# Performance work log

Measured on AMD Instinct MI355X. Metric: run time of the kernel, lower is better.

## Reference

```python
import jax, jax.numpy as jnp
import numpy as np
import math

D = 128  # hidden_dim
N_USERS = 10000
N_ITEMS = 12000
NEG_INF = -9e15


def setup_inputs() -> dict:
    key = jax.random.key(0)
    k1, k2, k3, k4, k5 = jax.random.split(key, 5)
    ufea = jax.random.normal(k1, (N_USERS, D), dtype=jnp.float32)
    inter = jax.random.normal(k2, (N_ITEMS, D), dtype=jnp.float32)
    adj = jax.random.randint(k3, (N_USERS, N_ITEMS), 0, 2, dtype=jnp.int32)
    # linear layer params (torch default init approximated with scaled normals)
    W = jax.random.normal(k4, (D, D), dtype=jnp.float32) / jnp.sqrt(jnp.float32(D))
    b = jax.random.normal(k5, (D,), dtype=jnp.float32) * 0.01
    return {"ufea": ufea, "inter": inter, "adj": adj, "W": W, "b": b}


def _leaky_relu2(x):
    # nn.LeakyReLU(2): negative_slope = 2
    return jnp.where(x > 0, x, 2.0 * x)


def reference(ufea, inter, adj, W, b):
    # GAT.forward_user with dropout in eval mode (identity).
    # Attention.forward(a=ufea, b=inter, adj)
    query = ufea @ W.T + b                      # [N, D]  nn.Linear
    scale = 1.0 / math.sqrt(D)
    scores = _leaky_relu2((query @ inter.T) * scale)   # [N, M]
    scores = jnp.where(adj > 0, scores, NEG_INF)        # mask non-edges
    attn = jax.nn.softmax(scores, axis=1)               # row softmax
    result = attn @ inter                                # [N, D]
    return result
```

## Files before the change

kernel.cpp:

```cpp
#include <hip/hip_runtime.h>
#include <cstdint>
#include <cstddef>


#define N_USERS 10000
#define N_ITEMS 12000
#define HD      128
#define QROWS   10112
#define NCHUNK  9
#define TILE    64
#define NTILES  188
#define UBLOCKS 79
#define QBLOCKS 632

typedef __bf16 bf16x8 __attribute__((ext_vector_type(8)));
typedef __bf16 bf16x4 __attribute__((ext_vector_type(4)));
typedef float  f32x4  __attribute__((ext_vector_type(4)));
typedef int    i32x4  __attribute__((ext_vector_type(4)));

typedef const __attribute__((address_space(1))) unsigned int g_u32;
typedef __attribute__((address_space(3))) unsigned int l_u32;

__global__ __launch_bounds__(256) void prep_kernel(const float* __restrict__ inter,
                                                   const float* __restrict__ ufea,
                                                   const float* __restrict__ W,
                                                   const float* __restrict__ bias,
                                                   __bf16* __restrict__ kvg,
                                                   __bf16* __restrict__ qg) {
    __shared__ __bf16 Tl[128 * 72];
    const int t = threadIdx.x;
    const int lane = t & 63, wave = t >> 6;
    const int n = lane & 15, qd = lane >> 4;

    if (blockIdx.x < NTILES) {
        const int tile = blockIdx.x;
        const int i0 = tile * 64;
        for (int it = 0; it < 8; ++it) {
            int g   = it * 256 + t;
            int row = g >> 5;
            int d   = (g & 31) * 4;
            int item = i0 + row;
            if (item < N_ITEMS) {
                f32x4 v = *(const f32x4*)(inter + (size_t)item * HD + d);
                Tl[(d + 0) * 72 + row] = (__bf16)v.x;
                Tl[(d + 1) * 72 + row] = (__bf16)v.y;
                Tl[(d + 2) * 72 + row] = (__bf16)v.z;
                Tl[(d + 3) * 72 + row] = (__bf16)v.w;
            } else {
                Tl[(d + 0) * 72 + row] = (__bf16)0.f;
                Tl[(d + 1) * 72 + row] = (__bf16)0.f;
                Tl[(d + 2) * 72 + row] = (__bf16)0.f;
                Tl[(d + 3) * 72 + row] = (__bf16)0.f;
            }
        }
        __syncthreads();
        __bf16* tbase = kvg + (size_t)tile * (32 * 512);
        #pragma unroll
        for (int j = 0; j < 4; ++j) {
            const int c = wave * 4 + j;
            int row = i0 + 4 * n + wave;
            bf16x8 o;
            if (row < N_ITEMS) {
                const float* p = inter + (size_t)row * HD + j * 32 + qd * 8;
                f32x4 lo = *(const f32x4*)p, hi = *(const f32x4*)(p + 4);
                o[0]=(__bf16)lo.x; o[1]=(__bf16)lo.y; o[2]=(__bf16)lo.z; o[3]=(__bf16)lo.w;
                o[4]=(__bf16)hi.x; o[5]=(__bf16)hi.y; o[6]=(__bf16)hi.z; o[7]=(__bf16)hi.w;
            } else {
                #pragma unroll
                for (int e = 0; e < 8; ++e) o[e] = (__bf16)0.f;
            }
            *(bf16x8*)(tbase + (size_t)c * 512 + lane * 8) = o;
        }
        #pragma unroll
        for (int j = 0; j < 4; ++j) {
            const int cc = wave * 4 + j;
            const int dt = cc >> 1, kc = cc & 1;
            bf16x8 v = *(const bf16x8*)&Tl[(dt * 16 + n) * 72 + kc * 32 + qd * 8];
            *(bf16x8*)(tbase + (size_t)(16 + cc) * 512 + lane * 8) = v;
        }
    } else {
        const int user0 = (blockIdx.x - NTILES) * 16;
        int arow = user0 + n; if (arow > N_USERS - 1) arow = N_USERS - 1;

        bf16x8 af[4];
        #pragma unroll
        for (int kk = 0; kk < 4; ++kk) {
            const float* p = ufea + (size_t)arow * HD + kk * 32 + qd * 8;
            f32x4 lo = *(const f32x4*)p, hi = *(const f32x4*)(p + 4);
            bf16x8 a;
            a[0]=(__bf16)lo.x; a[1]=(__bf16)lo.y; a[2]=(__bf16)lo.z; a[3]=(__bf16)lo.w;
            a[4]=(__bf16)hi.x; a[5]=(__bf16)hi.y; a[6]=(__bf16)hi.z; a[7]=(__bf16)hi.w;
            af[kk] = a;
        }
        #pragma unroll
        for (int h = 0; h < 2; ++h) {
            const int nt = wave * 2 + h;
            f32x4 acc = {0.f, 0.f, 0.f, 0.f};
            #pragma unroll
            for (int kk = 0; kk < 4; ++kk) {
                const float* p = W + (size_t)(nt * 16 + n) * HD + kk * 32 + qd * 8;
                f32x4 lo = *(const f32x4*)p, hi = *(const f32x4*)(p + 4);
                bf16x8 b;
                b[0]=(__bf16)lo.x; b[1]=(__bf16)lo.y; b[2]=(__bf16)lo.z; b[3]=(__bf16)lo.w;
                b[4]=(__bf16)hi.x; b[5]=(__bf16)hi.y; b[6]=(__bf16)hi.z; b[7]=(__bf16)hi.w;
                acc = __builtin_amdgcn_mfma_f32_16x16x32_bf16(af[kk], b, acc, 0, 0, 0);
            }
            const float bv = bias[nt * 16 + n];
            #pragma unroll
            for (int r = 0; r < 4; ++r) {
                int row = user0 + qd * 4 + r;
                qg[(size_t)row * HD + nt * 16 + n] = (__bf16)(acc[r] + bv);
            }
        }
    }
}

__global__ __launch_bounds__(256)
__attribute__((amdgpu_waves_per_eu(3)))
void fused_kernel(const __bf16* __restrict__ qg,
                  const __bf16* __restrict__ kvg,
                  const int* __restrict__ adj,
                  float* __restrict__ Opart,
                  float* __restrict__ lpart) {
    __shared__ __bf16 Kbuf[16 * 512];
    __shared__ __bf16 Vbuf[16 * 512];
    __shared__ __bf16 Pl[4][32 * 72];
    const int lane = threadIdx.x & 63, wave = threadIdx.x >> 6;
    const int n = lane & 15, qd = lane >> 4;
    const int user0 = blockIdx.y * 128 + wave * 32;
    const int chunk = blockIdx.x;
    const int t0 = (chunk * NTILES) / NCHUNK;
    const int t1 = ((chunk + 1) * NTILES) / NCHUNK;
    const float SC = (float)(1.4426950408889634 * 0.08838834764831845);

    bf16x8 qf[2][4];
    #pragma unroll
    for (int g = 0; g < 2; ++g)
        #pragma unroll
        for (int kk = 0; kk < 4; ++kk)
            qf[g][kk] = *(const bf16x8*)(qg + (size_t)(user0 + g * 16 + n) * HD + kk * 32 + qd * 8);

    f32x4 Oacc[2][8];
    #pragma unroll
    for (int g = 0; g < 2; ++g)
        #pragma unroll
        for (int dt = 0; dt < 8; ++dt) Oacc[g][dt] = (f32x4){0.f, 0.f, 0.f, 0.f};
    float lacc[2][4] = {{0.f,0.f,0.f,0.f},{0.f,0.f,0.f,0.f}};

    int adjOff[2][4];
    #pragma unroll
    for (int g = 0; g < 2; ++g)
        #pragma unroll
        for (int r = 0; r < 4; ++r) {
            int u = user0 + g * 16 + qd * 4 + r;
            if (u > N_USERS - 1) u = N_USERS - 1;
            adjOff[g][r] = u * N_ITEMS;
        }
    __bf16* pw = &Pl[wave][0];

    for (int T = t0; T < t1; ++T) {
        const int j0 = T * TILE;
        const __bf16* tb = kvg + (size_t)T * (32 * 512);

        __builtin_amdgcn_s_barrier();

        #pragma unroll
        for (int j = 0; j < 4; ++j) {
            const int c = wave * 4 + j;
            __builtin_amdgcn_global_load_lds((g_u32*)(tb + (size_t)c * 512 + lane * 8),
                                             (l_u32*)(&Kbuf[c * 512]), 16, 0, 0);
        }
        #pragma unroll
        for (int j = 0; j < 4; ++j) {
            const int c = wave * 4 + j;
            __builtin_amdgcn_global_load_lds((g_u32*)(tb + (size_t)(16 + c) * 512 + lane * 8),
                                             (l_u32*)(&Vbuf[c * 512]), 16, 0, 0);
        }
        i32x4 av[2][4];
        {
            int col4 = j0 + 4 * n;
            if (col4 > N_ITEMS - 4) col4 = N_ITEMS - 4;
            #pragma unroll
            for (int g = 0; g < 2; ++g)
                #pragma unroll
                for (int r = 0; r < 4; ++r)
                    av[g][r] = __builtin_nontemporal_load((const i32x4*)(adj + adjOff[g][r] + col4));
        }
        __syncthreads();

        unsigned m0 = 0, m1 = 0;
        #pragma unroll
        for (int r = 0; r < 4; ++r)
            #pragma unroll
            for (int nt = 0; nt < 4; ++nt) {
                m0 |= (unsigned)(av[0][r][nt] > 0) << (r * 4 + nt);
                m1 |= (unsigned)(av[1][r][nt] > 0) << (r * 4 + nt);
            }
        unsigned vnib = 0;
        #pragma unroll
        for (int nt = 0; nt < 4; ++nt)
            vnib |= (unsigned)(j0 + 4 * n + nt < N_ITEMS) << nt;
        const unsigned vrep = vnib * 0x1111u;
        m0 &= vrep; m1 &= vrep;

        #pragma unroll
        for (int g = 0; g < 2; ++g) {
            f32x4 S[4];
            #pragma unroll
            for (int nt = 0; nt < 4; ++nt) S[nt] = (f32x4){0.f, 0.f, 0.f, 0.f};
            #pragma unroll
            for (int nt = 0; nt < 4; ++nt) {
                #pragma unroll
                for (int kk = 0; kk < 4; ++kk) {
                    bf16x8 b = *(const bf16x8*)(&Kbuf[(nt * 4 + kk) * 512 + lane * 8]);
                    S[nt] = __builtin_amdgcn_mfma_f32_16x16x32_bf16(qf[g][kk], b, S[nt], 0, 0, 0);
                }
            }
            const unsigned mg = g ? m1 : m0;
            #pragma unroll
            for (int r = 0; r < 4; ++r) {
                bf16x4 pk;
                #pragma unroll
                for (int nt = 0; nt < 4; ++nt) {
                    float s = S[nt][r] * SC;
                    s = fminf(s, s + s);
                    const bool on = (mg >> (r * 4 + nt)) & 1u;
                    float p = on ? __builtin_amdgcn_exp2f(s) : 0.f;
                    lacc[g][r] += p;
                    pk[nt] = (__bf16)p;
                }
                *(bf16x4*)(pw + (g * 16 + qd * 4 + r) * 72 + 4 * n) = pk;
            }
        }

        #pragma unroll
        for (int kc = 0; kc < 2; ++kc) {
            bf16x8 af0 = *(const bf16x8*)(pw + (0 * 16 + n) * 72 + kc * 32 + qd * 8);
            bf16x8 af1 = *(const bf16x8*)(pw + (1 * 16 + n) * 72 + kc * 32 + qd * 8);
            #pragma unroll
            for (int dt = 0; dt < 8; ++dt) {
                bf16x8 b = *(const bf16x8*)(&Vbuf[(dt * 2 + kc) * 512 + lane * 8]);
                Oacc[0][dt] = __builtin_amdgcn_mfma_f32_16x16x32_bf16(af0, b, Oacc[0][dt], 0, 0, 0);
                Oacc[1][dt] = __builtin_amdgcn_mfma_f32_16x16x32_bf16(af1, b, Oacc[1][dt], 0, 0, 0);
            }
        }
    }

    #pragma unroll
    for (int g = 0; g < 2; ++g)
        #pragma unroll
        for (int r = 0; r < 4; ++r) {
            float v = lacc[g][r];
            v += __shfl_xor(v, 1);
            v += __shfl_xor(v, 2);
            v += __shfl_xor(v, 4);
            v += __shfl_xor(v, 8);
            lacc[g][r] = v;
        }
    const size_t cb = (size_t)chunk * QROWS;
    #pragma unroll
    for (int g = 0; g < 2; ++g)
        #pragma unroll
        for (int r = 0; r < 4; ++r) {
            const int user = user0 + g * 16 + qd * 4 + r;
            if (user < N_USERS) {
                #pragma unroll
                for (int dt = 0; dt < 8; ++dt)
                    Opart[(cb + user) * HD + dt * 16 + n] = Oacc[g][dt][r];
                if (n == 0) lpart[cb + user] = lacc[g][r];
            }
        }
}

__global__ __launch_bounds__(256) void combine_kernel(const float* __restrict__ Opart,
                                                      const float* __restrict__ lpart,
                                                      float* __restrict__ out) {
    const int g = blockIdx.x * 256 + threadIdx.x;
    const int base = g * 4;
    const int user = base >> 7;
    const int d = base & 127;
    f32x4 acc = {0.f, 0.f, 0.f, 0.f};
    float l = 0.f;
    #pragma unroll
    for (int c = 0; c < NCHUNK; ++c) {
        acc += *(const f32x4*)(Opart + ((size_t)c * QROWS + user) * HD + d);
        l += lpart[(size_t)c * QROWS + user];
    }
    if (user < N_USERS) {
        f32x4 res = acc / l;
        *(f32x4*)(out + (size_t)user * HD + d) = res;
    }
}

extern "C" void kernel_launch(void* const* d_in, const int* in_sizes, int n_in,
                              void* d_out, int out_size, void* d_ws, size_t ws_size,
                              hipStream_t stream) {
    const float* ufea = (const float*)d_in[0];
    const float* inter = (const float*)d_in[1];
    const int*   adj  = (const int*)d_in[2];
    const float* W    = (const float*)d_in[3];
    const float* bias = (const float*)d_in[4];
    float* out = (float*)d_out;

    char* ws = (char*)d_ws;
    __bf16* kvg  = (__bf16*)(ws);
    __bf16* qg   = (__bf16*)(ws + 6160384);
    float*  Opart = (float*)(ws + 8749056);
    float*  lpart = (float*)(ws + 55345152);

    prep_kernel<<<dim3(NTILES + QBLOCKS), dim3(256), 0, stream>>>(inter, ufea, W, bias, kvg, qg);
    fused_kernel<<<dim3(NCHUNK, UBLOCKS), dim3(256), 0, stream>>>(qg, kvg, adj, Opart, lpart);
    combine_kernel<<<dim3(1264), dim3(256), 0, stream>>>(Opart, lpart, out);
}
```

Before: 655.5 us.

## Enlarge fused blocks to 12 waves and double-buffer K/V tiles in LDS

```diff
diff --git a/kernel.cpp b/kernel.cpp
--- a/kernel.cpp
+++ b/kernel.cpp
@@ -6,12 +6,14 @@
 #define N_USERS 10000
 #define N_ITEMS 12000
 #define HD      128
-#define QROWS   10112
+#define QROWS   10368
 #define NCHUNK  9
 #define TILE    64
 #define NTILES  188
-#define UBLOCKS 79
-#define QBLOCKS 632
+#define UBLOCKS 27
+#define UB_USERS 384
+#define QBLOCKS 648
+#define WAVES   12
 
 typedef __bf16 bf16x8 __attribute__((ext_vector_type(8)));
 typedef __bf16 bf16x4 __attribute__((ext_vector_type(4)));
@@ -115,19 +117,19 @@
     }
 }
 
-__global__ __launch_bounds__(256)
+__global__ __launch_bounds__(768)
 __attribute__((amdgpu_waves_per_eu(3)))
 void fused_kernel(const __bf16* __restrict__ qg,
                   const __bf16* __restrict__ kvg,
                   const int* __restrict__ adj,
                   float* __restrict__ Opart,
                   float* __restrict__ lpart) {
-    __shared__ __bf16 Kbuf[16 * 512];
-    __shared__ __bf16 Vbuf[16 * 512];
-    __shared__ __bf16 Pl[4][32 * 72];
+    __shared__ __bf16 K0[16 * 512], K1[16 * 512];
+    __shared__ __bf16 V0[16 * 512], V1[16 * 512];
+    __shared__ __bf16 Pl[WAVES][32 * 72];
     const int lane = threadIdx.x & 63, wave = threadIdx.x >> 6;
     const int n = lane & 15, qd = lane >> 4;
-    const int user0 = blockIdx.y * 128 + wave * 32;
+    const int user0 = blockIdx.y * UB_USERS + wave * 32;
     const int chunk = blockIdx.x;
     const int t0 = (chunk * NTILES) / NCHUNK;
     const int t1 = ((chunk + 1) * NTILES) / NCHUNK;
@@ -158,24 +160,39 @@
         }
     __bf16* pw = &Pl[wave][0];
 
+    auto stage = [&](int T, bool toB) {
+        const __bf16* tb = kvg + (size_t)T * (32 * 512);
+        if (wave < 4) {
+            __bf16* dst = toB ? K1 : K0;
+            #pragma unroll
+            for (int j = 0; j < 4; ++j) {
+                const int c = wave * 4 + j;
+                __builtin_amdgcn_global_load_lds((g_u32*)(tb + (size_t)c * 512 + lane * 8),
+                                                 (l_u32*)(dst + c * 512), 16, 0, 0);
+            }
+        } else if (wave < 8) {
+            __bf16* dst = toB ? V1 : V0;
+            const int w4 = wave - 4;
+            #pragma unroll
+            for (int j = 0; j < 4; ++j) {
+                const int c = w4 * 4 + j;
+                __builtin_amdgcn_global_load_lds((g_u32*)(tb + (size_t)(16 + c) * 512 + lane * 8),
+                                                 (l_u32*)(dst + c * 512), 16, 0, 0);
+            }
+        }
+    };
+
+    stage(t0, false);
+    __syncthreads();
+
     for (int T = t0; T < t1; ++T) {
         const int j0 = T * TILE;
-        const __bf16* tb = kvg + (size_t)T * (32 * 512);
-
-        __builtin_amdgcn_s_barrier();
-
-        #pragma unroll
-        for (int j = 0; j < 4; ++j) {
-            const int c = wave * 4 + j;
-            __builtin_amdgcn_global_load_lds((g_u32*)(tb + (size_t)c * 512 + lane * 8),
-                                             (l_u32*)(&Kbuf[c * 512]), 16, 0, 0);
-        }
-        #pragma unroll
-        for (int j = 0; j < 4; ++j) {
-            const int c = wave * 4 + j;
-            __builtin_amdgcn_global_load_lds((g_u32*)(tb + (size_t)(16 + c) * 512 + lane * 8),
-                                             (l_u32*)(&Vbuf[c * 512]), 16, 0, 0);
-        }
+        const bool curB = ((T - t0) & 1) != 0;
+        const __bf16* kb = curB ? K1 : K0;
+        const __bf16* vb = curB ? V1 : V0;
+
+        if (T + 1 < t1) stage(T + 1, !curB);
+
         i32x4 av[2][4];
         {
             int col4 = j0 + 4 * n;
@@ -186,22 +203,12 @@
                 for (int r = 0; r < 4; ++r)
                     av[g][r] = __builtin_nontemporal_load((const i32x4*)(adj + adjOff[g][r] + col4));
         }
-        __syncthreads();
-
-        unsigned m0 = 0, m1 = 0;
-        #pragma unroll
-        for (int r = 0; r < 4; ++r)
-            #pragma unroll
-            for (int nt = 0; nt < 4; ++nt) {
-                m0 |= (unsigned)(av[0][r][nt] > 0) << (r * 4 + nt);
-                m1 |= (unsigned)(av[1][r][nt] > 0) << (r * 4 + nt);
-            }
+
         unsigned vnib = 0;
         #pragma unroll
         for (int nt = 0; nt < 4; ++nt)
             vnib |= (unsigned)(j0 + 4 * n + nt < N_ITEMS) << nt;
         const unsigned vrep = vnib * 0x1111u;
-        m0 &= vrep; m1 &= vrep;
 
         #pragma unroll
         for (int g = 0; g < 2; ++g) {
@@ -212,11 +219,17 @@
             for (int nt = 0; nt < 4; ++nt) {
                 #pragma unroll
                 for (int kk = 0; kk < 4; ++kk) {
-                    bf16x8 b = *(const bf16x8*)(&Kbuf[(nt * 4 + kk) * 512 + lane * 8]);
+                    bf16x8 b = *(const bf16x8*)(kb + (nt * 4 + kk) * 512 + lane * 8);
                     S[nt] = __builtin_amdgcn_mfma_f32_16x16x32_bf16(qf[g][kk], b, S[nt], 0, 0, 0);
                 }
             }
-            const unsigned mg = g ? m1 : m0;
+            unsigned mg = 0;
+            #pragma unroll
+            for (int r = 0; r < 4; ++r)
+                #pragma unroll
+                for (int nt = 0; nt < 4; ++nt)
+                    mg |= (unsigned)(av[g][r][nt] > 0) << (r * 4 + nt);
+            mg &= vrep;
             #pragma unroll
             for (int r = 0; r < 4; ++r) {
                 bf16x4 pk;
@@ -239,11 +252,13 @@
             bf16x8 af1 = *(const bf16x8*)(pw + (1 * 16 + n) * 72 + kc * 32 + qd * 8);
             #pragma unroll
             for (int dt = 0; dt < 8; ++dt) {
-                bf16x8 b = *(const bf16x8*)(&Vbuf[(dt * 2 + kc) * 512 + lane * 8]);
+                bf16x8 b = *(const bf16x8*)(vb + (dt * 2 + kc) * 512 + lane * 8);
                 Oacc[0][dt] = __builtin_amdgcn_mfma_f32_16x16x32_bf16(af0, b, Oacc[0][dt], 0, 0, 0);
                 Oacc[1][dt] = __builtin_amdgcn_mfma_f32_16x16x32_bf16(af1, b, Oacc[1][dt], 0, 0, 0);
             }
         }
+
+        __syncthreads();
     }
 
     #pragma unroll
@@ -305,10 +320,10 @@
     char* ws = (char*)d_ws;
     __bf16* kvg  = (__bf16*)(ws);
     __bf16* qg   = (__bf16*)(ws + 6160384);
-    float*  Opart = (float*)(ws + 8749056);
-    float*  lpart = (float*)(ws + 55345152);
+    float*  Opart = (float*)(ws + 8814592);
+    float*  lpart = (float*)(ws + 56590336);
 
     prep_kernel<<<dim3(NTILES + QBLOCKS), dim3(256), 0, stream>>>(inter, ufea, W, bias, kvg, qg);
-    fused_kernel<<<dim3(NCHUNK, UBLOCKS), dim3(256), 0, stream>>>(qg, kvg, adj, Opart, lpart);
-    combine_kernel<<<dim3(1264), dim3(256), 0, stream>>>(Opart, lpart, out);
+    fused_kernel<<<dim3(NCHUNK, UBLOCKS), dim3(768), 0, stream>>>(qg, kvg, adj, Opart, lpart);
+    combine_kernel<<<dim3(1296), dim3(256), 0, stream>>>(Opart, lpart, out);
 }
```

Result: slower. 773.3 us (+18.0%).

## Raise per-wave user rows to 48 and fold softmax scale into query

Applied to the files above, without the earlier changes.

```diff
diff --git a/kernel.cpp b/kernel.cpp
--- a/kernel.cpp
+++ b/kernel.cpp
@@ -6,12 +6,13 @@
 #define N_USERS 10000
 #define N_ITEMS 12000
 #define HD      128
-#define QROWS   10112
+#define QROWS   10176
 #define NCHUNK  9
 #define TILE    64
 #define NTILES  188
-#define UBLOCKS 79
-#define QBLOCKS 632
+#define UBLOCKS 53
+#define UB_USERS 192
+#define QBLOCKS 636
 
 typedef __bf16 bf16x8 __attribute__((ext_vector_type(8)));
 typedef __bf16 bf16x4 __attribute__((ext_vector_type(4)));
@@ -31,6 +32,7 @@
     const int t = threadIdx.x;
     const int lane = t & 63, wave = t >> 6;
     const int n = lane & 15, qd = lane >> 4;
+    const float SC = (float)(1.4426950408889634 * 0.08838834764831845);
 
     if (blockIdx.x < NTILES) {
         const int tile = blockIdx.x;
@@ -109,14 +111,13 @@
             #pragma unroll
             for (int r = 0; r < 4; ++r) {
                 int row = user0 + qd * 4 + r;
-                qg[(size_t)row * HD + nt * 16 + n] = (__bf16)(acc[r] + bv);
+                qg[(size_t)row * HD + nt * 16 + n] = (__bf16)((acc[r] + bv) * SC);
             }
         }
     }
 }
 
-__global__ __launch_bounds__(256)
-__attribute__((amdgpu_waves_per_eu(3)))
+__global__ __launch_bounds__(256, 2)
 void fused_kernel(const __bf16* __restrict__ qg,
                   const __bf16* __restrict__ kvg,
                   const int* __restrict__ adj,
@@ -124,32 +125,31 @@
                   float* __restrict__ lpart) {
     __shared__ __bf16 Kbuf[16 * 512];
     __shared__ __bf16 Vbuf[16 * 512];
-    __shared__ __bf16 Pl[4][32 * 72];
+    __shared__ __bf16 Pl[4][48 * 72];
     const int lane = threadIdx.x & 63, wave = threadIdx.x >> 6;
     const int n = lane & 15, qd = lane >> 4;
-    const int user0 = blockIdx.y * 128 + wave * 32;
+    const int user0 = blockIdx.y * UB_USERS + wave * 48;
     const int chunk = blockIdx.x;
     const int t0 = (chunk * NTILES) / NCHUNK;
     const int t1 = ((chunk + 1) * NTILES) / NCHUNK;
-    const float SC = (float)(1.4426950408889634 * 0.08838834764831845);
-
-    bf16x8 qf[2][4];
-    #pragma unroll
-    for (int g = 0; g < 2; ++g)
+
+    bf16x8 qf[3][4];
+    #pragma unroll
+    for (int g = 0; g < 3; ++g)
         #pragma unroll
         for (int kk = 0; kk < 4; ++kk)
             qf[g][kk] = *(const bf16x8*)(qg + (size_t)(user0 + g * 16 + n) * HD + kk * 32 + qd * 8);
 
-    f32x4 Oacc[2][8];
-    #pragma unroll
-    for (int g = 0; g < 2; ++g)
+    f32x4 Oacc[3][8];
+    #pragma unroll
+    for (int g = 0; g < 3; ++g)
         #pragma unroll
         for (int dt = 0; dt < 8; ++dt) Oacc[g][dt] = (f32x4){0.f, 0.f, 0.f, 0.f};
-    float lacc[2][4] = {{0.f,0.f,0.f,0.f},{0.f,0.f,0.f,0.f}};
-
-    int adjOff[2][4];
-    #pragma unroll
-    for (int g = 0; g < 2; ++g)
+    float lacc[3][4] = {{0.f,0.f,0.f,0.f},{0.f,0.f,0.f,0.f},{0.f,0.f,0.f,0.f}};
+
+    int adjOff[3][4];
+    #pragma unroll
+    for (int g = 0; g < 3; ++g)
         #pragma unroll
         for (int r = 0; r < 4; ++r) {
             int u = user0 + g * 16 + qd * 4 + r;
@@ -176,53 +176,59 @@
             __builtin_amdgcn_global_load_lds((g_u32*)(tb + (size_t)(16 + c) * 512 + lane * 8),
                                              (l_u32*)(&Vbuf[c * 512]), 16, 0, 0);
         }
-        i32x4 av[2][4];
+        i32x4 av[3][4];
         {
             int col4 = j0 + 4 * n;
             if (col4 > N_ITEMS - 4) col4 = N_ITEMS - 4;
             #pragma unroll
-            for (int g = 0; g < 2; ++g)
+            for (int g = 0; g < 3; ++g)
                 #pragma unroll
                 for (int r = 0; r < 4; ++r)
                     av[g][r] = __builtin_nontemporal_load((const i32x4*)(adj + adjOff[g][r] + col4));
         }
         __syncthreads();
 
-        unsigned m0 = 0, m1 = 0;
+        unsigned m0 = 0, m1 = 0, m2 = 0;
         #pragma unroll
         for (int r = 0; r < 4; ++r)
             #pragma unroll
             for (int nt = 0; nt < 4; ++nt) {
                 m0 |= (unsigned)(av[0][r][nt] > 0) << (r * 4 + nt);
                 m1 |= (unsigned)(av[1][r][nt] > 0) << (r * 4 + nt);
+                m2 |= (unsigned)(av[2][r][nt] > 0) << (r * 4 + nt);
             }
         unsigned vnib = 0;
         #pragma unroll
         for (int nt = 0; nt < 4; ++nt)
             vnib |= (unsigned)(j0 + 4 * n + nt < N_ITEMS) << nt;
         const unsigned vrep = vnib * 0x1111u;
-        m0 &= vrep; m1 &= vrep;
-
-        #pragma unroll
-        for (int g = 0; g < 2; ++g) {
-            f32x4 S[4];
-            #pragma unroll
-            for (int nt = 0; nt < 4; ++nt) S[nt] = (f32x4){0.f, 0.f, 0.f, 0.f};
-            #pragma unroll
-            for (int nt = 0; nt < 4; ++nt) {
-                #pragma unroll
-                for (int kk = 0; kk < 4; ++kk) {
-                    bf16x8 b = *(const bf16x8*)(&Kbuf[(nt * 4 + kk) * 512 + lane * 8]);
-                    S[nt] = __builtin_amdgcn_mfma_f32_16x16x32_bf16(qf[g][kk], b, S[nt], 0, 0, 0);
-                }
-            }
-            const unsigned mg = g ? m1 : m0;
+        m0 &= vrep; m1 &= vrep; m2 &= vrep;
+
+        f32x4 S[3][4];
+        #pragma unroll
+        for (int g = 0; g < 3; ++g)
+            #pragma unroll
+            for (int nt = 0; nt < 4; ++nt) S[g][nt] = (f32x4){0.f, 0.f, 0.f, 0.f};
+        #pragma unroll
+        for (int nt = 0; nt < 4; ++nt) {
+            #pragma unroll
+            for (int kk = 0; kk < 4; ++kk) {
+                bf16x8 b = *(const bf16x8*)(&Kbuf[(nt * 4 + kk) * 512 + lane * 8]);
+                S[0][nt] = __builtin_amdgcn_mfma_f32_16x16x32_bf16(qf[0][kk], b, S[0][nt], 0, 0, 0);
+                S[1][nt] = __builtin_amdgcn_mfma_f32_16x16x32_bf16(qf[1][kk], b, S[1][nt], 0, 0, 0);
+                S[2][nt] = __builtin_amdgcn_mfma_f32_16x16x32_bf16(qf[2][kk], b, S[2][nt], 0, 0, 0);
+            }
+        }
+
+        #pragma unroll
+        for (int g = 0; g < 3; ++g) {
+            const unsigned mg = (g == 0) ? m0 : (g == 1) ? m1 : m2;
             #pragma unroll
             for (int r = 0; r < 4; ++r) {
                 bf16x4 pk;
                 #pragma unroll
                 for (int nt = 0; nt < 4; ++nt) {
-                    float s = S[nt][r] * SC;
+                    float s = S[g][nt][r];
                     s = fminf(s, s + s);
                     const bool on = (mg >> (r * 4 + nt)) & 1u;
                     float p = on ? __builtin_amdgcn_exp2f(s) : 0.f;
@@ -237,17 +243,19 @@
         for (int kc = 0; kc < 2; ++kc) {
             bf16x8 af0 = *(const bf16x8*)(pw + (0 * 16 + n) * 72 + kc * 32 + qd * 8);
             bf16x8 af1 = *(const bf16x8*)(pw + (1 * 16 + n) * 72 + kc * 32 + qd * 8);
+            bf16x8 af2 = *(const bf16x8*)(pw + (2 * 16 + n) * 72 + kc * 32 + qd * 8);
             #pragma unroll
             for (int dt = 0; dt < 8; ++dt) {
                 bf16x8 b = *(const bf16x8*)(&Vbuf[(dt * 2 + kc) * 512 + lane * 8]);
                 Oacc[0][dt] = __builtin_amdgcn_mfma_f32_16x16x32_bf16(af0, b, Oacc[0][dt], 0, 0, 0);
                 Oacc[1][dt] = __builtin_amdgcn_mfma_f32_16x16x32_bf16(af1, b, Oacc[1][dt], 0, 0, 0);
+                Oacc[2][dt] = __builtin_amdgcn_mfma_f32_16x16x32_bf16(af2, b, Oacc[2][dt], 0, 0, 0);
             }
         }
     }
 
     #pragma unroll
-    for (int g = 0; g < 2; ++g)
+    for (int g = 0; g < 3; ++g)
         #pragma unroll
         for (int r = 0; r < 4; ++r) {
             float v = lacc[g][r];
@@ -259,7 +267,7 @@
         }
     const size_t cb = (size_t)chunk * QROWS;
     #pragma unroll
-    for (int g = 0; g < 2; ++g)
+    for (int g = 0; g < 3; ++g)
         #pragma unroll
         for (int r = 0; r < 4; ++r) {
             const int user = user0 + g * 16 + qd * 4 + r;
@@ -305,10 +313,10 @@
     char* ws = (char*)d_ws;
     __bf16* kvg  = (__bf16*)(ws);
     __bf16* qg   = (__bf16*)(ws + 6160384);
-    float*  Opart = (float*)(ws + 8749056);
-    float*  lpart = (float*)(ws + 55345152);
+    float*  Opart = (float*)(ws + 8765440);
+    float*  lpart = (float*)(ws + 55656448);
 
     prep_kernel<<<dim3(NTILES + QBLOCKS), dim3(256), 0, stream>>>(inter, ufea, W, bias, kvg, qg);
     fused_kernel<<<dim3(NCHUNK, UBLOCKS), dim3(256), 0, stream>>>(qg, kvg, adj, Opart, lpart);
-    combine_kernel<<<dim3(1264), dim3(256), 0, stream>>>(Opart, lpart, out);
+    combine_kernel<<<dim3(1250), dim3(256), 0, stream>>>(Opart, lpart, out);
 }
```

After: 720.9 us. +10.0%, slower.
